# Kernel tuning notes

Hardware: AMD Instinct MI355X
Metric: run time of the kernel (lower is better)

## Reference

```python
import jax, jax.numpy as jnp
import numpy as np

N, F, F_, H = 8192, 128, 64, 4
NEG = -1e10  # K.constant(-10000000000.0) mask value


def setup_inputs() -> dict:
    key = jax.random.key(0)
    k1, k2, k3, k4, k5 = jax.random.split(key, 5)
    X = jax.random.normal(k1, (N, F), dtype=jnp.float32)
    A = jax.random.randint(k2, (N, N), 0, 2).astype(jnp.float32)
    W = jax.random.normal(k3, (H, F, F_), dtype=jnp.float32) * 0.1
    a_self = jax.random.normal(k4, (H, F_), dtype=jnp.float32) * 0.1
    a_neigh = jax.random.normal(k5, (H, F_), dtype=jnp.float32) * 0.1
    return {"X": X, "A": A, "W": W, "a_self": a_self, "a_neigh": a_neigh}


def reference(X, A, W, a_self, a_neigh):
    # per-head linear projection: [H, N, F_]
    Xp = jnp.einsum('nf,hfd->hnd', X, W)
    # additive attention scores
    s_self = jnp.einsum('hnd,hd->hn', Xp, a_self)    # [H, N]
    s_neigh = jnp.einsum('hnd,hd->hn', Xp, a_neigh)  # [H, N]
    dense = s_self[:, :, None] + s_neigh[:, None, :]  # [H, N, N]
    dense = jnp.where(dense > 0, dense, 0.2 * dense)  # LeakyReLU(0.2)
    mask = jnp.where(A == 0.0, jnp.float32(NEG), jnp.float32(0.0))  # [N, N]
    attn = jax.nn.softmax(dense + mask[None], axis=-1)  # [H, N, N]
    # dropout on attention coeffs is identity at inference
    feats = jnp.einsum('hnm,hmd->hnd', attn, Xp)  # [H, N, F_]
    feats = jax.nn.relu(feats)  # activation applied per head before concat
    # concat heads -> [N, H*F_]
    return jnp.transpose(feats, (1, 0, 2)).reshape(N, H * F_)
```

## Files before the change

kernel.cpp:

```cpp
#include <hip/hip_runtime.h>
#include <stdint.h>


#define NN    8192
#define FF    128
#define FD    64
#define HH    4
#define SPLIT 8
#define KT_PER_SPLIT ((NN / SPLIT) / 32)
#define LOG2E 1.4426950408889634f

typedef __attribute__((ext_vector_type(8))) short short8;
typedef __attribute__((ext_vector_type(4))) float f32x4;

extern "C" __device__ float __ocml_exp2_f32(float);

__device__ __forceinline__ float fast_exp2(float x) {
#if __has_builtin(__builtin_amdgcn_exp2f)
    return __builtin_amdgcn_exp2f(x);
#else
    return __ocml_exp2_f32(x);
#endif
}

__device__ __forceinline__ float bf16_to_f32(unsigned short u) {
    return __builtin_bit_cast(float, ((unsigned)u) << 16);
}
__device__ __forceinline__ unsigned f32_to_bf16_rne(float f) {
    unsigned u = __builtin_bit_cast(unsigned, f);
    u = (u + 0x7FFFu + ((u >> 16) & 1u)) >> 16;
    return u;
}
__device__ __forceinline__ unsigned pack_bf16_trunc(float lo, float hi) {
    return __builtin_amdgcn_perm(__builtin_bit_cast(unsigned, hi),
                                 __builtin_bit_cast(unsigned, lo), 0x07060302u);
}
__device__ __forceinline__ void async_load16(const void* g, void* l) {
    __builtin_amdgcn_global_load_lds(
        (const __attribute__((address_space(1))) unsigned int*)g,
        (__attribute__((address_space(3))) unsigned int*)l, 16, 0, 0);
}
__device__ __forceinline__ unsigned enc_key(float f) {
    unsigned u = __builtin_bit_cast(unsigned, f);
    return (u & 0x80000000u) ? ~u : (u | 0x80000000u);
}
__device__ __forceinline__ float dec_key(unsigned k) {
    unsigned u = (k & 0x80000000u) ? (k ^ 0x80000000u) : ~k;
    return __builtin_bit_cast(float, u);
}

#define WS_XPT   0
#define WS_U     (WS_XPT + HH * FD * NN * 2)
#define WS_V     (WS_U + HH * NN * 4)
#define WS_MK    (WS_V + HH * NN * 4)
#define WS_WT    (WS_MK + 256)
#define WS_ACCP  (WS_WT + HH * FD * FF * 2)
#define WS_LP    (WS_ACCP + (size_t)SPLIT * HH * NN * FD * 2)

__global__ void k0_transpose_w(const float* __restrict__ W,
                               unsigned short* __restrict__ WT,
                               unsigned* __restrict__ MK) {
    int b = blockIdx.x;
    int t = threadIdx.x;
    if (b == 0 && t < 8) MK[t] = 0u;
    int h = b >> 3, fb = b & 7;
    int d = t & 63, fo = t >> 6;
    #pragma unroll
    for (int i = 0; i < 4; ++i) {
        int f = fb * 16 + fo * 4 + i;
        WT[(h * FD + d) * FF + f] = (unsigned short)f32_to_bf16_rne(W[(h * FF + f) * FD + d]);
    }
}

__global__ __launch_bounds__(256) void k1_project(
        const float* __restrict__ X,
        const unsigned short* __restrict__ WT,
        const float* __restrict__ a_self,
        const float* __restrict__ a_neigh,
        unsigned short* __restrict__ XpT,
        float* __restrict__ U, float* __restrict__ V,
        unsigned* __restrict__ MK) {
    __shared__ __align__(16) char XsB[64 * 272];
    __shared__ __align__(16) char WsB[64 * 272];
    const int rb = blockIdx.x * 64;
    const int h  = blockIdx.y;
    const int t  = threadIdx.x;
    const float4* xs = (const float4*)(X + (size_t)rb * FF);
    #pragma unroll
    for (int i = 0; i < 8; ++i) {
        int c = i * 256 + t;
        float4 v = xs[c];
        uint2 pv;
        pv.x = f32_to_bf16_rne(v.x) | (f32_to_bf16_rne(v.y) << 16);
        pv.y = f32_to_bf16_rne(v.z) | (f32_to_bf16_rne(v.w) << 16);
        *(uint2*)(XsB + (c >> 5) * 272 + (c & 31) * 8) = pv;
    }
    const uint4* wsrc = (const uint4*)(WT + (size_t)h * FD * FF);
    #pragma unroll
    for (int i = 0; i < 4; ++i) {
        int c = i * 256 + t;
        *(uint4*)(WsB + (c >> 4) * 272 + (c & 15) * 16) = wsrc[c];
    }
    __syncthreads();
    const int lane = t & 63, wid = t >> 6;
    const int r15 = lane & 15, quad = lane >> 4;
    const int lrow = wid * 16 + r15;

    f32x4 acc[4];
    #pragma unroll
    for (int cg = 0; cg < 4; ++cg) acc[cg] = (f32x4){0.f, 0.f, 0.f, 0.f};
    #pragma unroll
    for (int kt = 0; kt < 4; ++kt) {
        short8 afr = *(const short8*)(XsB + lrow * 272 + kt * 64 + quad * 16);
        #pragma unroll
        for (int cg = 0; cg < 4; ++cg) {
            short8 bfr = *(const short8*)(WsB + (cg * 16 + r15) * 272 + kt * 64 + quad * 16);
            acc[cg] = __builtin_amdgcn_mfma_f32_16x16x32_bf16(afr, bfr, acc[cg], 0, 0, 0);
        }
    }
    float as[4], an[4];
    #pragma unroll
    for (int cg = 0; cg < 4; ++cg) {
        as[cg] = a_self[h * FD + cg * 16 + r15];
        an[cg] = a_neigh[h * FD + cg * 16 + r15];
    }
    float mu = -1e30f, mv = -1e30f;
    #pragma unroll
    for (int reg = 0; reg < 4; ++reg) {
        float s1 = 0.f, s2 = 0.f;
        #pragma unroll
        for (int cg = 0; cg < 4; ++cg) { s1 += acc[cg][reg] * as[cg]; s2 += acc[cg][reg] * an[cg]; }
        #pragma unroll
        for (int m = 1; m <= 8; m <<= 1) { s1 += __shfl_xor(s1, m); s2 += __shfl_xor(s2, m); }
        mu = fmaxf(mu, s1); mv = fmaxf(mv, s2);
        if (r15 == 0) {
            int n = rb + wid * 16 + quad * 4 + reg;
            U[h * NN + n] = s1;
            V[h * NN + n] = s2;
        }
    }
    mu = fmaxf(mu, __shfl_xor(mu, 16)); mu = fmaxf(mu, __shfl_xor(mu, 32));
    mv = fmaxf(mv, __shfl_xor(mv, 16)); mv = fmaxf(mv, __shfl_xor(mv, 32));
    if (lane == 0) {
        atomicMax(&MK[h], enc_key(mu));
        atomicMax(&MK[4 + h], enc_key(mv));
    }
    #pragma unroll
    for (int cg = 0; cg < 4; ++cg) {
        uint2 val;
        val.x = f32_to_bf16_rne(acc[cg][0]) | (f32_to_bf16_rne(acc[cg][1]) << 16);
        val.y = f32_to_bf16_rne(acc[cg][2]) | (f32_to_bf16_rne(acc[cg][3]) << 16);
        int d = cg * 16 + r15;
        int n0 = rb + wid * 16 + quad * 4;
        *(uint2*)((char*)XpT + ((size_t)(h * FD + d) * NN + n0) * 2) = val;
    }
}

__global__ __launch_bounds__(256, 3) void k2_attend(
        const float* __restrict__ Ag,
        const unsigned short* __restrict__ XpT,
        const float* __restrict__ U, const float* __restrict__ V,
        const unsigned* __restrict__ MK,
        unsigned short* __restrict__ accP,
        float* __restrict__ lP) {
    __shared__ __align__(16) char Xsb[2][16384];
    __shared__ __align__(16) char Asb[2][8192];
    const int t = threadIdx.x;
    const int lane = t & 63, wid = t >> 6;
    const int r15 = lane & 15, quad = lane >> 4;
    const int rb = blockIdx.x * 64;
    const int sp = blockIdx.y;
    const int h = wid;
    const int kb0 = sp * (NN / SPLIT);

    const float M = dec_key(MK[h]) + dec_key(MK[4 + h]);
    const float qoff = -0.8f * M * LOG2E;
    float u1g[4];
    #pragma unroll
    for (int g = 0; g < 4; ++g)
        u1g[g] = (U[h * NN + rb + g * 16 + r15] - M) * LOG2E;

    f32x4 acc[4][4];
    #pragma unroll
    for (int g = 0; g < 4; ++g)
        #pragma unroll
        for (int cg = 0; cg < 4; ++cg) acc[g][cg] = (f32x4){0.f, 0.f, 0.f, 0.f};
    float lsum[4] = {0.f, 0.f, 0.f, 0.f};

    const int srX = wid * 64 + (lane >> 2);
    const int scX = (lane & 3) ^ ((lane >> 3) & 3);
    const char* xsrc = (const char*)XpT + ((size_t)srX * NN + kb0 + scX * 8) * 2;
    const size_t xstep = (size_t)16 * NN * 2;
    const int rA = wid * 16 + (lane >> 3);
    const int chA = (lane & 7) ^ (((rA >> 1) & 3) << 1);
    const float* asrc = Ag + (size_t)(rb + rA) * NN + kb0 + chA * 4;
    const size_t astep = (size_t)8 * NN;

    #pragma unroll
    for (int i = 0; i < 4; ++i)
        async_load16(xsrc + (size_t)i * xstep, &Xsb[0][(wid * 4 + i) * 1024]);
    #pragma unroll
    for (int i = 0; i < 2; ++i)
        async_load16(asrc + i * astep, &Asb[0][(wid * 2 + i) * 1024]);

    const float* vbase = V + h * NN + kb0 + quad * 8;
    float4 vg[2][2];
    vg[0][0] = *(const float4*)(vbase);
    vg[0][1] = *(const float4*)(vbase + 4);

    const int swzX = (quad ^ ((r15 >> 1) & 3)) * 16;
    const int swzA = (quad ^ ((r15 >> 1) & 3)) * 32;

    #pragma unroll 2
    for (int kt = 0; kt < KT_PER_SPLIT; ++kt) {
        const int cur = kt & 1, nxt = cur ^ 1;
        __syncthreads();
        if (kt + 1 < KT_PER_SPLIT) {
            const char*  xs2 = xsrc + (size_t)(kt + 1) * 64;
            const float* as2 = asrc + (size_t)(kt + 1) * 32;
            #pragma unroll
            for (int i = 0; i < 4; ++i)
                async_load16(xs2 + (size_t)i * xstep, &Xsb[nxt][(wid * 4 + i) * 1024]);
            #pragma unroll
            for (int i = 0; i < 2; ++i)
                async_load16(as2 + i * astep, &Asb[nxt][(wid * 2 + i) * 1024]);
        }
        {
            const int ktn = (kt + 1 < KT_PER_SPLIT) ? kt + 1 : kt;
            vg[nxt][0] = *(const float4*)(vbase + ktn * 32);
            vg[nxt][1] = *(const float4*)(vbase + ktn * 32 + 4);
        }
        short8 bfr[4];
        #pragma unroll
        for (int cg = 0; cg < 4; ++cg)
            bfr[cg] = *(const short8*)(&Xsb[cur][(h * FD + cg * 16 + r15) * 64 + swzX]);

        #pragma unroll
        for (int g = 0; g < 4; ++g) {
            const char* arow = &Asb[cur][(g * 16 + r15) * 128 + swzA];
            f32x4 a0 = *(const f32x4*)(arow);
            f32x4 a1 = *(const f32x4*)(arow + 16);
            float w[8];
            #pragma unroll
            for (int j = 0; j < 4; ++j) {
                float p = fmaf(((const float*)&vg[cur][0])[j], LOG2E, u1g[g]);
                float q = fmaf(0.2f, p, qoff);
                w[j] = fast_exp2(fmaxf(p, q)) * a0[j];
            }
            #pragma unroll
            for (int j = 0; j < 4; ++j) {
                float p = fmaf(((const float*)&vg[cur][1])[j], LOG2E, u1g[g]);
                float q = fmaf(0.2f, p, qoff);
                w[4 + j] = fast_exp2(fmaxf(p, q)) * a1[j];
            }
            lsum[g] += ((w[0] + w[1]) + (w[2] + w[3])) + ((w[4] + w[5]) + (w[6] + w[7]));
            uint4 pkv;
            pkv.x = pack_bf16_trunc(w[0], w[1]);
            pkv.y = pack_bf16_trunc(w[2], w[3]);
            pkv.z = pack_bf16_trunc(w[4], w[5]);
            pkv.w = pack_bf16_trunc(w[6], w[7]);
            short8 afrag = __builtin_bit_cast(short8, pkv);
            #pragma unroll
            for (int cg = 0; cg < 4; ++cg)
                acc[g][cg] = __builtin_amdgcn_mfma_f32_16x16x32_bf16(afrag, bfr[cg], acc[g][cg], 0, 0, 0);
        }
    }
    #pragma unroll
    for (int g = 0; g < 4; ++g) {
        lsum[g] += __shfl_xor(lsum[g], 16);
        lsum[g] += __shfl_xor(lsum[g], 32);
    }
    if (lane < 16) {
        #pragma unroll
        for (int g = 0; g < 4; ++g)
            lP[(size_t)(sp * HH + h) * NN + rb + g * 16 + lane] = lsum[g];
    }
    #pragma unroll
    for (int g = 0; g < 4; ++g)
        #pragma unroll
        for (int cg = 0; cg < 4; ++cg) {
            int d = cg * 16 + r15;
            #pragma unroll
            for (int reg = 0; reg < 4; ++reg) {
                int n = rb + g * 16 + quad * 4 + reg;
                accP[((size_t)(sp * HH + h) * NN + n) * FD + d] =
                    (unsigned short)f32_to_bf16_rne(acc[g][cg][reg]);
            }
        }
}

__global__ void k3_combine(const unsigned short* __restrict__ accP,
                           const float* __restrict__ lP,
                           float* __restrict__ out) {
    int e = blockIdx.x * 256 + threadIdx.x;
    int n = e >> 8, c = e & 255;
    int h = c >> 6, d = c & 63;
    float num = 0.f, den = 0.f;
    #pragma unroll
    for (int s = 0; s < SPLIT; ++s) {
        num += bf16_to_f32(accP[((size_t)(s * HH + h) * NN + n) * FD + d]);
        den += lP[(size_t)(s * HH + h) * NN + n];
    }
    out[e] = fmaxf(num * __builtin_amdgcn_rcpf(den), 0.f);
}

extern "C" void kernel_launch(void* const* d_in, const int* in_sizes, int n_in,
                              void* d_out, int out_size, void* d_ws, size_t ws_size,
                              hipStream_t stream) {
    (void)in_sizes; (void)n_in; (void)out_size; (void)ws_size;
    const float* X       = (const float*)d_in[0];
    const float* A       = (const float*)d_in[1];
    const float* W       = (const float*)d_in[2];
    const float* a_self  = (const float*)d_in[3];
    const float* a_neigh = (const float*)d_in[4];
    char* ws = (char*)d_ws;
    unsigned short* XpT  = (unsigned short*)(ws + WS_XPT);
    float*          U    = (float*)(ws + WS_U);
    float*          V    = (float*)(ws + WS_V);
    unsigned*       MK   = (unsigned*)(ws + WS_MK);
    unsigned short* WT   = (unsigned short*)(ws + WS_WT);
    unsigned short* accP = (unsigned short*)(ws + WS_ACCP);
    float*          lP   = (float*)(ws + WS_LP);
    float*          out  = (float*)d_out;

    k0_transpose_w<<<dim3(32), dim3(256), 0, stream>>>(W, WT, MK);
    k1_project<<<dim3(NN / 64, HH), dim3(256), 0, stream>>>(X, WT, a_self, a_neigh, XpT, U, V, MK);
    k2_attend<<<dim3(NN / 64, SPLIT), dim3(256), 0, stream>>>(A, XpT, U, V, MK, accP, lP);
    k3_combine<<<dim3(NN), dim3(256), 0, stream>>>(accP, lP, out);
}
```

Baseline: 506.2 us.

## Precompute adjacency bitmask and drop fp32 A tiles from attention kernel

A new pre-pass kernel streams the fp32 adjacency matrix once and uses wave ballots to pack it into a 32-bit-per-word bitmask. The attention kernel then reads mask words straight into registers and zeroes masked exponentials with a bitwise AND instead of multiplying by A. This removes the A staging buffers from LDS and allows raising the occupancy hint from 3 to 4 blocks. The full A read still happens, but now in a separate serial kernel rather than overlapped with the attention compute, so that traffic is no longer hidden behind the math.

```diff
diff --git a/kernel.cpp b/kernel.cpp
--- a/kernel.cpp
+++ b/kernel.cpp
@@ -40,6 +40,13 @@
         (const __attribute__((address_space(1))) unsigned int*)g,
         (__attribute__((address_space(3))) unsigned int*)l, 16, 0, 0);
 }
+__device__ __forceinline__ unsigned bit_mask32(unsigned v, int j) {
+#if __has_builtin(__builtin_amdgcn_sbfe)
+    return (unsigned)__builtin_amdgcn_sbfe((int)v, j, 1);
+#else
+    return (unsigned)(-(int)((v >> j) & 1u));
+#endif
+}
 __device__ __forceinline__ unsigned enc_key(float f) {
     unsigned u = __builtin_bit_cast(unsigned, f);
     return (u & 0x80000000u) ? ~u : (u | 0x80000000u);
@@ -56,6 +63,23 @@
 #define WS_WT    (WS_MK + 256)
 #define WS_ACCP  (WS_WT + HH * FD * FF * 2)
 #define WS_LP    (WS_ACCP + (size_t)SPLIT * HH * NN * FD * 2)
+#define WS_M32   (WS_LP + (size_t)SPLIT * HH * NN * 4)
+
+__global__ __launch_bounds__(256) void ka_bitmask(const float* __restrict__ Ag,
+                                                  unsigned* __restrict__ M32) {
+    const int lane = threadIdx.x & 63;
+    const size_t wave_id = (size_t)((blockIdx.x * 256 + threadIdx.x) >> 6);
+    const size_t stride = (size_t)8192 * 64;
+    size_t base = wave_id * 64;
+    #pragma unroll 4
+    for (int s = 0; s < 128; ++s) {
+        float a = Ag[base + lane];
+        unsigned long long m = __ballot(a != 0.0f);
+        if (lane == 0)
+            *(unsigned long long*)(M32 + (base >> 5)) = m;
+        base += stride;
+    }
+}
 
 __global__ void k0_transpose_w(const float* __restrict__ W,
                                unsigned short* __restrict__ WT,
@@ -156,15 +180,14 @@
     }
 }
 
-__global__ __launch_bounds__(256, 3) void k2_attend(
-        const float* __restrict__ Ag,
+__global__ __launch_bounds__(256, 4) void k2_attend(
+        const unsigned* __restrict__ M32,
         const unsigned short* __restrict__ XpT,
         const float* __restrict__ U, const float* __restrict__ V,
         const unsigned* __restrict__ MK,
         unsigned short* __restrict__ accP,
         float* __restrict__ lP) {
     __shared__ __align__(16) char Xsb[2][16384];
-    __shared__ __align__(16) char Asb[2][8192];
     const int t = threadIdx.x;
     const int lane = t & 63, wid = t >> 6;
     const int r15 = lane & 15, quad = lane >> 4;
@@ -191,45 +214,35 @@
     const int scX = (lane & 3) ^ ((lane >> 3) & 3);
     const char* xsrc = (const char*)XpT + ((size_t)srX * NN + kb0 + scX * 8) * 2;
     const size_t xstep = (size_t)16 * NN * 2;
-    const int rA = wid * 16 + (lane >> 3);
-    const int chA = (lane & 7) ^ (((rA >> 1) & 3) << 1);
-    const float* asrc = Ag + (size_t)(rb + rA) * NN + kb0 + chA * 4;
-    const size_t astep = (size_t)8 * NN;
-
     #pragma unroll
     for (int i = 0; i < 4; ++i)
         async_load16(xsrc + (size_t)i * xstep, &Xsb[0][(wid * 4 + i) * 1024]);
-    #pragma unroll
-    for (int i = 0; i < 2; ++i)
-        async_load16(asrc + i * astep, &Asb[0][(wid * 2 + i) * 1024]);
+
+    const unsigned* mbase = M32 + (size_t)(rb + r15) * 256 + sp * 32;
+    unsigned mg[2][4];
+    #pragma unroll
+    for (int g = 0; g < 4; ++g) mg[0][g] = mbase[g * 16 * 256];
 
     const float* vbase = V + h * NN + kb0 + quad * 8;
-    float4 vg[2][2];
-    vg[0][0] = *(const float4*)(vbase);
-    vg[0][1] = *(const float4*)(vbase + 4);
-
     const int swzX = (quad ^ ((r15 >> 1) & 3)) * 16;
-    const int swzA = (quad ^ ((r15 >> 1) & 3)) * 32;
 
     #pragma unroll 2
     for (int kt = 0; kt < KT_PER_SPLIT; ++kt) {
         const int cur = kt & 1, nxt = cur ^ 1;
         __syncthreads();
         if (kt + 1 < KT_PER_SPLIT) {
-            const char*  xs2 = xsrc + (size_t)(kt + 1) * 64;
-            const float* as2 = asrc + (size_t)(kt + 1) * 32;
+            const char* xs2 = xsrc + (size_t)(kt + 1) * 64;
             #pragma unroll
             for (int i = 0; i < 4; ++i)
                 async_load16(xs2 + (size_t)i * xstep, &Xsb[nxt][(wid * 4 + i) * 1024]);
             #pragma unroll
-            for (int i = 0; i < 2; ++i)
-                async_load16(as2 + i * astep, &Asb[nxt][(wid * 2 + i) * 1024]);
-        }
-        {
-            const int ktn = (kt + 1 < KT_PER_SPLIT) ? kt + 1 : kt;
-            vg[nxt][0] = *(const float4*)(vbase + ktn * 32);
-            vg[nxt][1] = *(const float4*)(vbase + ktn * 32 + 4);
-        }
+            for (int g = 0; g < 4; ++g) mg[nxt][g] = mbase[g * 16 * 256 + kt + 1];
+        } else {
+            #pragma unroll
+            for (int g = 0; g < 4; ++g) mg[nxt][g] = mg[cur][g];
+        }
+        f32x4 va  = *(const f32x4*)(vbase + kt * 32);
+        f32x4 vb2 = *(const f32x4*)(vbase + kt * 32 + 4);
         short8 bfr[4];
         #pragma unroll
         for (int cg = 0; cg < 4; ++cg)
@@ -237,21 +250,23 @@
 
         #pragma unroll
         for (int g = 0; g < 4; ++g) {
-            const char* arow = &Asb[cur][(g * 16 + r15) * 128 + swzA];
-            f32x4 a0 = *(const f32x4*)(arow);
-            f32x4 a1 = *(const f32x4*)(arow + 16);
+            const unsigned mbits = mg[cur][g] >> (quad * 8);
             float w[8];
             #pragma unroll
             for (int j = 0; j < 4; ++j) {
-                float p = fmaf(((const float*)&vg[cur][0])[j], LOG2E, u1g[g]);
+                float p = fmaf(va[j], LOG2E, u1g[g]);
                 float q = fmaf(0.2f, p, qoff);
-                w[j] = fast_exp2(fmaxf(p, q)) * a0[j];
+                float e = fast_exp2(fmaxf(p, q));
+                w[j] = __builtin_bit_cast(float,
+                         __builtin_bit_cast(unsigned, e) & bit_mask32(mbits, j));
             }
             #pragma unroll
             for (int j = 0; j < 4; ++j) {
-                float p = fmaf(((const float*)&vg[cur][1])[j], LOG2E, u1g[g]);
+                float p = fmaf(vb2[j], LOG2E, u1g[g]);
                 float q = fmaf(0.2f, p, qoff);
-                w[4 + j] = fast_exp2(fmaxf(p, q)) * a1[j];
+                float e = fast_exp2(fmaxf(p, q));
+                w[4 + j] = __builtin_bit_cast(float,
+                         __builtin_bit_cast(unsigned, e) & bit_mask32(mbits, 4 + j));
             }
             lsum[g] += ((w[0] + w[1]) + (w[2] + w[3])) + ((w[4] + w[5]) + (w[6] + w[7]));
             uint4 pkv;
@@ -321,10 +336,12 @@
     unsigned short* WT   = (unsigned short*)(ws + WS_WT);
     unsigned short* accP = (unsigned short*)(ws + WS_ACCP);
     float*          lP   = (float*)(ws + WS_LP);
+    unsigned*       M32  = (unsigned*)(ws + WS_M32);
     float*          out  = (float*)d_out;
 
+    ka_bitmask<<<dim3(2048), dim3(256), 0, stream>>>(A, M32);
     k0_transpose_w<<<dim3(32), dim3(256), 0, stream>>>(W, WT, MK);
     k1_project<<<dim3(NN / 64, HH), dim3(256), 0, stream>>>(X, WT, a_self, a_neigh, XpT, U, V, MK);
-    k2_attend<<<dim3(NN / 64, SPLIT), dim3(256), 0, stream>>>(A, XpT, U, V, MK, accP, lP);
+    k2_attend<<<dim3(NN / 64, SPLIT), dim3(256), 0, stream>>>(M32, XpT, U, V, MK, accP, lP);
     k3_combine<<<dim3(NN), dim3(256), 0, stream>>>(accP, lP, out);
 }
```

Measured after the change: 648.4 us. 28.1% more time.
